# Kernel tuning notes

Measured on AMD Instinct MI355X. Metric: run time of the kernel, lower is better.

## Reference

```python
import jax, jax.numpy as jnp
import numpy as np

B, C, H, W = 2, 256, 64, 64
FEAT = 256          # in_channels * expansion_ratio
HEADS = 8
HS = FEAT // HEADS  # 32
OUT = 256


def setup_inputs() -> dict:
    key = jax.random.key(0)
    ks = jax.random.split(key, 12)
    inp = {
        "x": jax.random.normal(ks[0], (B, C, H, W), jnp.float32),
        "mod_multiplier": jax.random.normal(ks[1], (B, FEAT), jnp.float32),
        "mod_bias": jax.random.normal(ks[2], (B, FEAT), jnp.float32),
        # learned parameters (1x1 convs as matrices)
        "w_qkv": jax.random.normal(ks[3], (3 * FEAT, C), jnp.float32) * 0.02,
        "b_qkv": jnp.zeros((3 * FEAT,), jnp.float32),
        "w_proj": jax.random.normal(ks[4], (OUT, FEAT), jnp.float32) * 0.02,
        "pe_q_h": jax.random.normal(ks[5], (1, FEAT, H, 1), jnp.float32) * 0.02,
        "pe_q_w": jax.random.normal(ks[6], (1, FEAT, 1, W), jnp.float32) * 0.02,
        "pe_k_h": jax.random.normal(ks[7], (1, FEAT, H, 1), jnp.float32) * 0.02,
        "pe_k_w": jax.random.normal(ks[8], (1, FEAT, 1, W), jnp.float32) * 0.02,
        "pre_act_bias": jnp.zeros((1, C, 1, 1), jnp.float32),
        "pre_qkv_bias": jnp.zeros((1, C, 1, 1), jnp.float32),
        "pre_proj_bias": jnp.zeros((1, FEAT, 1, 1), jnp.float32),
        "id_scale": jnp.ones((1, OUT, 1, 1), jnp.float32),
    }
    return inp


def reference(x, mod_multiplier, mod_bias, w_qkv, b_qkv, w_proj,
              pe_q_h, pe_q_w, pe_k_h, pe_k_w,
              pre_act_bias, pre_qkv_bias, pre_proj_bias, id_scale):
    b = x.shape[0]
    # pre-activation (Fixup-style biases)
    x_preact = jax.nn.silu(x + pre_act_bias) + pre_qkv_bias
    # 1x1 conv -> QKV: [b, 3F, H, W]
    qkv = jnp.einsum('bchw,oc->bohw', x_preact, w_qkv) + b_qkv[None, :, None, None]
    q, k, v = jnp.split(qkv, 3, axis=1)
    # additive positional embeddings
    q = q + pe_q_h + pe_q_w
    k = k + pe_k_h + pe_k_w
    # FiLM modulation of query
    q = q * mod_multiplier[:, :, None, None] + mod_bias[:, :, None, None]
    # [b, heads, head_size, H*W]
    q = q.reshape(b, HEADS, HS, H * W)
    k = k.reshape(b, HEADS, HS, H * W)
    v = v.reshape(b, HEADS, HS, H * W)
    scale = jnp.asarray(HS ** 0.5, x.dtype)
    logits = jnp.einsum('bhdn,bhdm->bhnm', q, k) / scale
    weights = jax.nn.softmax(logits, axis=-1)
    attn = jnp.einsum('bhnm,bhdm->bhdn', weights, v)
    attn = attn.reshape(b, FEAT, H, W)
    # output projection (1x1 conv, no bias)
    x_res = jnp.einsum('bchw,oc->bohw', attn + pre_proj_bias, w_proj)
    return x * id_scale + x_res
```

## Files before the change

kernel.cpp:

```cpp
#include <hip/hip_runtime.h>
#include <hip/hip_bf16.h>
#include <cstdint>

#define NB   2
#define NC   256
#define NN   4096
#define NH   8
#define HSZ  32
#define NF   256
#define N3F  768

typedef __bf16 bf16x8 __attribute__((ext_vector_type(8)));
typedef __bf16 bf16x4 __attribute__((ext_vector_type(4)));
typedef short  s16x4  __attribute__((ext_vector_type(4)));
typedef float  floatx4 __attribute__((ext_vector_type(4)));

#define QSCALE 0.25506601622184f

__global__ void k_prep(const float* __restrict__ x, const float* __restrict__ pab,
                       const float* __restrict__ pqb, __bf16* __restrict__ y,
                       const float* __restrict__ wqkv, const float* __restrict__ wproj,
                       __bf16* __restrict__ wqb, __bf16* __restrict__ wpb) {
    __shared__ __bf16 ct[32 * 264];
    int bid = blockIdx.x, tid = threadIdx.x;
    if (bid >= 256) {
        int id = (bid - 256) * 1024 + tid * 4;
        const float* src = (id < 196608) ? (wqkv + id) : (wproj + (id - 196608));
        __bf16* dst = (id < 196608) ? (wqb + id) : (wpb + (id - 196608));
        float4 v = *(const float4*)src;
        bf16x4 o;
        o[0] = (__bf16)v.x; o[1] = (__bf16)v.y; o[2] = (__bf16)v.z; o[3] = (__bf16)v.w;
        *(bf16x4*)dst = o;
        return;
    }
    int b = bid >> 7, nt = bid & 127;
    int n0 = nt * 32;
    int cbase = tid >> 3, nc = tid & 7;
#pragma unroll
    for (int q = 0; q < 8; q++) {
        int c = cbase + q * 32;
        const float4 xv = *(const float4*)(x + ((size_t)b * NC + c) * NN + n0 + nc * 4);
        float bias = pab[c], qb = pqb[c];
        float vs[4] = {xv.x, xv.y, xv.z, xv.w};
#pragma unroll
        for (int i = 0; i < 4; i++) {
            float s = vs[i] + bias;
            float r = s / (1.f + __expf(-s)) + qb;
            ct[(nc * 4 + i) * 264 + c] = (__bf16)r;
        }
    }
    __syncthreads();
#pragma unroll
    for (int q = 0; q < 4; q++) {
        int id = tid + q * 256;
        int n = id >> 5, ck = (id & 31) * 8;
        bf16x8 v = *(const bf16x8*)(ct + n * 264 + ck);
        *(bf16x8*)(y + ((size_t)b * NN + n0 + n) * NC + ck) = v;
    }
}

__launch_bounds__(256)
__global__ void k_qkv(const __bf16* __restrict__ y, const __bf16* __restrict__ wb,
                      const float* __restrict__ bqkv,
                      const float* __restrict__ peqh, const float* __restrict__ peqw,
                      const float* __restrict__ pekh, const float* __restrict__ pekw,
                      const float* __restrict__ mm, const float* __restrict__ mb,
                      __bf16* __restrict__ qs, __bf16* __restrict__ kf, __bf16* __restrict__ vf) {
    __shared__ __bf16 smem[4][64 * 40];
    __bf16* ct = &smem[0][0];
    const int nt = blockIdx.x, ot = blockIdx.y, b = blockIdx.z;
    const int tid = threadIdx.x;
    const int wave = tid >> 6, lane = tid & 63, ln = lane & 15, quad = lane >> 4;
    const int wm = (wave & 1) * 32, wn = (wave >> 1) * 32;
    floatx4 acc[2][2];
#pragma unroll
    for (int i = 0; i < 2; i++)
#pragma unroll
        for (int j = 0; j < 2; j++) acc[i][j] = 0.f;
    const __bf16* ysrc = y + ((size_t)b * NN + nt * 64) * NC;
    const __bf16* wsrc = wb + (size_t)ot * 64 * NC;
    const int r0 = tid >> 2, c0 = (tid & 3) * 8;
    bf16x8 ya = *(const bf16x8*)(ysrc + (size_t)r0 * NC + c0);
    bf16x8 wa = *(const bf16x8*)(wsrc + (size_t)r0 * NC + c0);
    for (int ko = 0; ko < 8; ko++) {
        int buf = ko & 1;
        *(bf16x8*)(&smem[buf][r0 * 40 + c0]) = ya;
        *(bf16x8*)(&smem[2 + buf][r0 * 40 + c0]) = wa;
        __syncthreads();
        if (ko < 7) {
            int kc = (ko + 1) * 32;
            ya = *(const bf16x8*)(ysrc + (size_t)r0 * NC + kc + c0);
            wa = *(const bf16x8*)(wsrc + (size_t)r0 * NC + kc + c0);
        }
        bf16x8 af[2], bfr[2];
#pragma unroll
        for (int ii = 0; ii < 2; ii++) af[ii]  = *(const bf16x8*)(&smem[buf][(wm + ii * 16 + ln) * 40 + quad * 8]);
#pragma unroll
        for (int jj = 0; jj < 2; jj++) bfr[jj] = *(const bf16x8*)(&smem[2 + buf][(wn + jj * 16 + ln) * 40 + quad * 8]);
#pragma unroll
        for (int ii = 0; ii < 2; ii++)
#pragma unroll
            for (int jj = 0; jj < 2; jj++)
                acc[ii][jj] = __builtin_amdgcn_mfma_f32_16x16x32_bf16(af[ii], bfr[jj], acc[ii][jj], 0, 0, 0);
    }
    __syncthreads();
    if (ot < 8) {
#pragma unroll
        for (int ii = 0; ii < 2; ii++)
#pragma unroll
            for (int jj = 0; jj < 2; jj++) {
                int o_l = wn + jj * 16 + ln;
                int o_g = ot * 64 + o_l;
                float bq = bqkv[o_g];
#pragma unroll
                for (int r = 0; r < 4; r++) {
                    int n_l = wm + ii * 16 + quad * 4 + r;
                    float val = acc[ii][jj][r] + bq;
                    if (ot < 4) {
                        val += peqh[o_g * 64 + nt] + peqw[o_g * 64 + n_l];
                        val = val * mm[b * NF + o_g] + mb[b * NF + o_g];
                        val *= QSCALE;
                    } else {
                        int c = o_g - 256;
                        val += pekh[c * 64 + nt] + pekw[c * 64 + n_l];
                    }
                    ct[n_l * 72 + o_l] = (__bf16)val;
                }
            }
        __syncthreads();
#pragma unroll
        for (int q = 0; q < 2; q++) {
            int id = tid + q * 256;
            int n_l = id >> 3, oc = (id & 7) * 8;
            bf16x8 v = *(const bf16x8*)(ct + n_l * 72 + oc);
            int n_g = nt * 64 + n_l;
            int o_g = ot * 64 + oc;
            if (ot < 4) {
                int h = o_g >> 5, d = o_g & 31;
                *(bf16x8*)(qs + (((size_t)b * NH + h) * NN + n_g) * HSZ + d) = v;
            } else {
                int c = o_g - 256, h = c >> 5, d0 = c & 31;
                size_t blk = ((size_t)(b * NH + h) * 256 + (n_g >> 4)) * 512;
                *(bf16x8*)(kf + blk + (d0 >> 3) * 128 + (n_g & 15) * 8) = v;
            }
        }
    } else {
#pragma unroll
        for (int ii = 0; ii < 2; ii++)
#pragma unroll
            for (int jj = 0; jj < 2; jj++) {
                int o_l = wn + jj * 16 + ln;
                float bq = bqkv[ot * 64 + o_l];
#pragma unroll
                for (int r = 0; r < 4; r++) {
                    int n_l = wm + ii * 16 + quad * 4 + r;
                    ct[o_l * 72 + n_l] = (__bf16)(acc[ii][jj][r] + bq);
                }
            }
        __syncthreads();
#pragma unroll
        for (int q = 0; q < 4; q++) {
            int id = tid + q * 256;
            int o_l = id >> 4, ng4 = (id & 15) * 4;
            bf16x4 v = *(const bf16x4*)(ct + o_l * 72 + ng4);
            int c = (ot - 8) * 64 + o_l, h = c >> 5, d = c & 31;
            int dj = d >> 4, lnv = d & 15;
            int m_g = nt * 64 + ng4;
            size_t blk = ((size_t)(b * NH + h) * 256 + (m_g >> 4)) * 512;
            *(bf16x4*)(vf + blk + (((m_g >> 2) & 3) * 16 + lnv) * 8 + dj * 4) = v;
        }
    }
}

__launch_bounds__(256)
__global__ void k_attn(const __bf16* __restrict__ qs, const __bf16* __restrict__ kf,
                       const __bf16* __restrict__ vf,
                       __bf16* __restrict__ po, float* __restrict__ pl) {
    __shared__ __bf16 sbuf[2 * 8192];
    int bi = blockIdx.x;
    int xcd = bi & 7, r = bi >> 3;
    int bh = xcd * 2 + (r & 1);
    int r2 = r >> 1;
    int qt = r2 & 31, half = r2 >> 5;
    int tid = threadIdx.x, wave = tid >> 6, lane = tid & 63, ln = lane & 15, quad = lane >> 4;
    int n0 = qt * 128 + wave * 32;
    const __bf16* qbase = qs + (size_t)bh * NN * HSZ;
    const __bf16* kfb = kf + ((size_t)bh * 256 + half * 128) * 512;
    const __bf16* vfb = vf + ((size_t)bh * 256 + half * 128) * 512;
    bf16x8 qa[2];
    qa[0] = *(const bf16x8*)(qbase + (size_t)(n0 + ln) * HSZ + quad * 8);
    qa[1] = *(const bf16x8*)(qbase + (size_t)(n0 + 16 + ln) * HSZ + quad * 8);
    floatx4 o[2][2], o2[2];
    o[0][0] = 0.f; o[0][1] = 0.f; o[1][0] = 0.f; o[1][1] = 0.f;
    o2[0] = 0.f; o2[1] = 0.f;
    floatx4 zf = 0.f;
    s16x4 ones;
    ones[0] = (short)0x3F80; ones[1] = (short)0x3F80;
    ones[2] = (short)0x3F80; ones[3] = (short)0x3F80;
    const int toff = tid * 8;
    const int lo = lane * 8;
    bf16x8 kr0, kr1, vr0, vr1;
    kr0 = *(const bf16x8*)(kfb + toff);
    kr1 = *(const bf16x8*)(kfb + toff + 2048);
    vr0 = *(const bf16x8*)(vfb + toff);
    vr1 = *(const bf16x8*)(vfb + toff + 2048);
    for (int mt = 0; mt < 16; mt++) {
        int bo = (mt & 1) << 13;
        *(bf16x8*)(sbuf + bo + toff) = kr0;
        *(bf16x8*)(sbuf + bo + toff + 2048) = kr1;
        *(bf16x8*)(sbuf + bo + 4096 + toff) = vr0;
        *(bf16x8*)(sbuf + bo + 4096 + toff + 2048) = vr1;
        __syncthreads();
        if (mt < 15) {
            const __bf16* kn = kfb + (mt + 1) * 4096;
            const __bf16* vn = vfb + (mt + 1) * 4096;
            kr0 = *(const bf16x8*)(kn + toff);
            kr1 = *(const bf16x8*)(kn + toff + 2048);
            vr0 = *(const bf16x8*)(vn + toff);
            vr1 = *(const bf16x8*)(vn + toff + 2048);
        }
        const __bf16* kl = sbuf + bo;
        const __bf16* vl = sbuf + bo + 4096;
#pragma unroll
        for (int j = 0; j < 8; j++) {
            bf16x8 kfr = *(const bf16x8*)(kl + j * 512 + lo);
            bf16x8 vfr = *(const bf16x8*)(vl + j * 512 + lo);
            s16x4 vb0, vb1;
            __builtin_memcpy(&vb0, &vfr, 8);
            __builtin_memcpy(&vb1, (const char*)&vfr + 8, 8);
#pragma unroll
            for (int i = 0; i < 2; i++) {
                floatx4 s = __builtin_amdgcn_mfma_f32_16x16x32_bf16(kfr, qa[i], zf, 0, 0, 0);
                bf16x4 p;
#pragma unroll
                for (int rr = 0; rr < 4; rr++)
                    p[rr] = (__bf16)__builtin_amdgcn_exp2f(s[rr]);
                s16x4 pa;
                __builtin_memcpy(&pa, &p, 8);
                o[i][0] = __builtin_amdgcn_mfma_f32_16x16x16bf16_1k(pa, vb0, o[i][0], 0, 0, 0);
                o[i][1] = __builtin_amdgcn_mfma_f32_16x16x16bf16_1k(pa, vb1, o[i][1], 0, 0, 0);
                o2[i]   = __builtin_amdgcn_mfma_f32_16x16x16bf16_1k(pa, ones, o2[i], 0, 0, 0);
            }
        }
    }
    size_t plbase = (size_t)(half * 16 + bh) * NN;
    if (ln == 0)
#pragma unroll
        for (int i = 0; i < 2; i++)
#pragma unroll
            for (int rr = 0; rr < 4; rr++)
                pl[plbase + n0 + i * 16 + quad * 4 + rr] = o2[i][rr];
    __bf16* ct = sbuf;
#pragma unroll
    for (int i = 0; i < 2; i++)
#pragma unroll
        for (int dj = 0; dj < 2; dj++)
#pragma unroll
            for (int rr = 0; rr < 4; rr++)
                ct[(wave * 32 + i * 16 + quad * 4 + rr) * 32 + dj * 16 + ln] = (__bf16)o[i][dj][rr];
    __syncthreads();
    size_t pobase = ((size_t)(half * 16 + bh) * NN + (size_t)qt * 128) * HSZ;
#pragma unroll
    for (int q = 0; q < 2; q++) {
        int id = tid + q * 256;
        int n_l = id >> 2, dc = (id & 3) * 8;
        *(bf16x8*)(po + pobase + n_l * HSZ + dc) = *(const bf16x8*)(ct + n_l * 32 + dc);
    }
}

__launch_bounds__(256)
__global__ void k_proj(const __bf16* __restrict__ po, const float* __restrict__ pl,
                       const __bf16* __restrict__ wpb, const float* __restrict__ ppb,
                       const float* __restrict__ x, const float* __restrict__ idsc,
                       float* __restrict__ out) {
    __shared__ __bf16 at[64 * 264];
    __shared__ __bf16 bt[2][64 * 40];
    __shared__ float linv[8 * 64];
    __shared__ float ppbs[256];
    int nt = blockIdx.x, ot = blockIdx.y, b = blockIdx.z;
    int tid = threadIdx.x, wave = tid >> 6, lane = tid & 63, ln = lane & 15, quad = lane >> 4;
    int wo = (wave & 1) * 32, wn = (wave >> 1) * 32;
#pragma unroll
    for (int q = 0; q < 8; q++) {
        int id = tid + q * 256;
        int row = id >> 5, fc = (id & 31) * 8;
        *(bf16x8*)(at + row * 264 + fc) = *(const bf16x8*)(wpb + (size_t)(ot * 64 + row) * NF + fc);
    }
#pragma unroll
    for (int q = 0; q < 2; q++) {
        int id = tid + q * 256;
        int h = id >> 6, n_l = id & 63;
        size_t base = (size_t)(b * NH + h) * NN + nt * 64 + n_l;
        linv[id] = 1.f / (pl[base] + pl[base + (size_t)16 * NN]);
    }
    ppbs[tid] = ppb[tid];
    __syncthreads();
    floatx4 acc[2][2];
#pragma unroll
    for (int i = 0; i < 2; i++)
#pragma unroll
        for (int j = 0; j < 2; j++) acc[i][j] = 0.f;
    const int n_l = tid >> 2, dh8 = (tid & 3) * 8;
    const size_t hstep = (size_t)NN * HSZ;
    const size_t half_off = (size_t)16 * NN * HSZ;
    size_t prow = ((size_t)b * NH * NN + (size_t)nt * 64 + n_l) * HSZ + dh8;
    bf16x8 p0 = *(const bf16x8*)(po + prow);
    bf16x8 p1 = *(const bf16x8*)(po + prow + half_off);
    for (int ko = 0; ko < 8; ko++) {
        int buf = ko & 1;
        float iv = linv[ko * 64 + n_l];
        bf16x8 c;
#pragma unroll
        for (int e = 0; e < 8; e++)
            c[e] = (__bf16)(((float)p0[e] + (float)p1[e]) * iv + ppbs[ko * 32 + dh8 + e]);
        *(bf16x8*)(&bt[buf][n_l * 40 + dh8]) = c;
        __syncthreads();
        if (ko < 7) {
            size_t pr = prow + (size_t)(ko + 1) * hstep;
            p0 = *(const bf16x8*)(po + pr);
            p1 = *(const bf16x8*)(po + pr + half_off);
        }
        bf16x8 af[2], bfr[2];
#pragma unroll
        for (int oi = 0; oi < 2; oi++) af[oi]  = *(const bf16x8*)(at + (wo + oi * 16 + ln) * 264 + ko * 32 + quad * 8);
#pragma unroll
        for (int nj = 0; nj < 2; nj++) bfr[nj] = *(const bf16x8*)(&bt[buf][(wn + nj * 16 + ln) * 40 + quad * 8]);
#pragma unroll
        for (int oi = 0; oi < 2; oi++)
#pragma unroll
            for (int nj = 0; nj < 2; nj++)
                acc[oi][nj] = __builtin_amdgcn_mfma_f32_16x16x32_bf16(af[oi], bfr[nj], acc[oi][nj], 0, 0, 0);
    }
#pragma unroll
    for (int oi = 0; oi < 2; oi++)
#pragma unroll
        for (int nj = 0; nj < 2; nj++)
#pragma unroll
            for (int r = 0; r < 4; r++) {
                int o_g = ot * 64 + wo + oi * 16 + quad * 4 + r;
                int n_g = nt * 64 + wn + nj * 16 + ln;
                size_t idx = ((size_t)b * NF + o_g) * NN + n_g;
                out[idx] = x[idx] * idsc[o_g] + acc[oi][nj][r];
            }
}

extern "C" void kernel_launch(void* const* d_in, const int* in_sizes, int n_in,
                              void* d_out, int out_size, void* d_ws, size_t ws_size,
                              hipStream_t stream) {
    (void)in_sizes; (void)n_in; (void)out_size; (void)ws_size;
    const float* x    = (const float*)d_in[0];
    const float* mm   = (const float*)d_in[1];
    const float* mb   = (const float*)d_in[2];
    const float* wqkv = (const float*)d_in[3];
    const float* bqkv = (const float*)d_in[4];
    const float* wproj= (const float*)d_in[5];
    const float* peqh = (const float*)d_in[6];
    const float* peqw = (const float*)d_in[7];
    const float* pekh = (const float*)d_in[8];
    const float* pekw = (const float*)d_in[9];
    const float* pab  = (const float*)d_in[10];
    const float* pqb  = (const float*)d_in[11];
    const float* ppb  = (const float*)d_in[12];
    const float* idsc = (const float*)d_in[13];
    float* out = (float*)d_out;

    __bf16* ws = (__bf16*)d_ws;
    const size_t SEG = 2097152;
    __bf16* y    = ws;
    __bf16* qs   = ws + SEG;
    __bf16* kf   = ws + SEG * 2;
    __bf16* vf   = ws + SEG * 3;
    __bf16* po   = ws + SEG * 4;
    float*  pl   = (float*)(ws + SEG * 6);
    __bf16* wqb  = ws + SEG * 6 + 262144;
    __bf16* wpb  = wqb + 196608;

    hipLaunchKernelGGL(k_prep, dim3(512), dim3(256), 0, stream,
                       x, pab, pqb, y, wqkv, wproj, wqb, wpb);
    hipLaunchKernelGGL(k_qkv,  dim3(64, 12, 2), dim3(256), 0, stream,
                       y, wqb, bqkv, peqh, peqw, pekh, pekw, mm, mb, qs, kf, vf);
    hipLaunchKernelGGL(k_attn, dim3(1024), dim3(256), 0, stream, qs, kf, vf, po, pl);
    hipLaunchKernelGGL(k_proj, dim3(64, 4, 2), dim3(256), 0, stream,
                       po, pl, wpb, ppb, x, idsc, out);
}
```

Measured before the change: 175.0 us.

## Shrink attention LDS tiles, sum softmax denominators on VALU, widen projection blocks

After: 175.8 us. No clear change (+0.4%).

```diff
diff --git a/kernel.cpp b/kernel.cpp
--- a/kernel.cpp
+++ b/kernel.cpp
@@ -83,9 +83,9 @@
     bf16x8 ya = *(const bf16x8*)(ysrc + (size_t)r0 * NC + c0);
     bf16x8 wa = *(const bf16x8*)(wsrc + (size_t)r0 * NC + c0);
     for (int ko = 0; ko < 8; ko++) {
-        int buf = ko & 1;
-        *(bf16x8*)(&smem[buf][r0 * 40 + c0]) = ya;
-        *(bf16x8*)(&smem[2 + buf][r0 * 40 + c0]) = wa;
+        int bo = ko & 1;
+        *(bf16x8*)(&smem[bo][r0 * 40 + c0]) = ya;
+        *(bf16x8*)(&smem[2 + bo][r0 * 40 + c0]) = wa;
         __syncthreads();
         if (ko < 7) {
             int kc = (ko + 1) * 32;
@@ -94,9 +94,9 @@
         }
         bf16x8 af[2], bfr[2];
 #pragma unroll
-        for (int ii = 0; ii < 2; ii++) af[ii]  = *(const bf16x8*)(&smem[buf][(wm + ii * 16 + ln) * 40 + quad * 8]);
-#pragma unroll
-        for (int jj = 0; jj < 2; jj++) bfr[jj] = *(const bf16x8*)(&smem[2 + buf][(wn + jj * 16 + ln) * 40 + quad * 8]);
+        for (int ii = 0; ii < 2; ii++) af[ii]  = *(const bf16x8*)(&smem[bo][(wm + ii * 16 + ln) * 40 + quad * 8]);
+#pragma unroll
+        for (int jj = 0; jj < 2; jj++) bfr[jj] = *(const bf16x8*)(&smem[2 + bo][(wn + jj * 16 + ln) * 40 + quad * 8]);
 #pragma unroll
         for (int ii = 0; ii < 2; ii++)
 #pragma unroll
@@ -172,11 +172,11 @@
     }
 }
 
-__launch_bounds__(256)
+__launch_bounds__(256, 6)
 __global__ void k_attn(const __bf16* __restrict__ qs, const __bf16* __restrict__ kf,
                        const __bf16* __restrict__ vf,
                        __bf16* __restrict__ po, float* __restrict__ pl) {
-    __shared__ __bf16 sbuf[2 * 8192];
+    __shared__ __bf16 sbuf[2 * 4096];
     int bi = blockIdx.x;
     int xcd = bi & 7, r = bi >> 3;
     int bh = xcd * 2 + (r & 1);
@@ -190,39 +190,28 @@
     bf16x8 qa[2];
     qa[0] = *(const bf16x8*)(qbase + (size_t)(n0 + ln) * HSZ + quad * 8);
     qa[1] = *(const bf16x8*)(qbase + (size_t)(n0 + 16 + ln) * HSZ + quad * 8);
-    floatx4 o[2][2], o2[2];
+    floatx4 o[2][2];
     o[0][0] = 0.f; o[0][1] = 0.f; o[1][0] = 0.f; o[1][1] = 0.f;
-    o2[0] = 0.f; o2[1] = 0.f;
+    floatx4 lsum4[2];
+    lsum4[0] = 0.f; lsum4[1] = 0.f;
     floatx4 zf = 0.f;
-    s16x4 ones;
-    ones[0] = (short)0x3F80; ones[1] = (short)0x3F80;
-    ones[2] = (short)0x3F80; ones[3] = (short)0x3F80;
     const int toff = tid * 8;
     const int lo = lane * 8;
-    bf16x8 kr0, kr1, vr0, vr1;
-    kr0 = *(const bf16x8*)(kfb + toff);
-    kr1 = *(const bf16x8*)(kfb + toff + 2048);
-    vr0 = *(const bf16x8*)(vfb + toff);
-    vr1 = *(const bf16x8*)(vfb + toff + 2048);
-    for (int mt = 0; mt < 16; mt++) {
-        int bo = (mt & 1) << 13;
-        *(bf16x8*)(sbuf + bo + toff) = kr0;
-        *(bf16x8*)(sbuf + bo + toff + 2048) = kr1;
-        *(bf16x8*)(sbuf + bo + 4096 + toff) = vr0;
-        *(bf16x8*)(sbuf + bo + 4096 + toff + 2048) = vr1;
-        __syncthreads();
-        if (mt < 15) {
-            const __bf16* kn = kfb + (mt + 1) * 4096;
-            const __bf16* vn = vfb + (mt + 1) * 4096;
-            kr0 = *(const bf16x8*)(kn + toff);
-            kr1 = *(const bf16x8*)(kn + toff + 2048);
-            vr0 = *(const bf16x8*)(vn + toff);
-            vr1 = *(const bf16x8*)(vn + toff + 2048);
+    bf16x8 kr = *(const bf16x8*)(kfb + toff);
+    bf16x8 vr = *(const bf16x8*)(vfb + toff);
+    for (int mt = 0; mt < 32; mt++) {
+        int bo = (mt & 1) << 12;
+        *(bf16x8*)(sbuf + bo + toff) = kr;
+        *(bf16x8*)(sbuf + bo + 2048 + toff) = vr;
+        __syncthreads();
+        if (mt < 31) {
+            kr = *(const bf16x8*)(kfb + (mt + 1) * 2048 + toff);
+            vr = *(const bf16x8*)(vfb + (mt + 1) * 2048 + toff);
         }
         const __bf16* kl = sbuf + bo;
-        const __bf16* vl = sbuf + bo + 4096;
-#pragma unroll
-        for (int j = 0; j < 8; j++) {
+        const __bf16* vl = sbuf + bo + 2048;
+#pragma unroll
+        for (int j = 0; j < 4; j++) {
             bf16x8 kfr = *(const bf16x8*)(kl + j * 512 + lo);
             bf16x8 vfr = *(const bf16x8*)(vl + j * 512 + lo);
             s16x4 vb0, vb1;
@@ -233,23 +222,26 @@
                 floatx4 s = __builtin_amdgcn_mfma_f32_16x16x32_bf16(kfr, qa[i], zf, 0, 0, 0);
                 bf16x4 p;
 #pragma unroll
-                for (int rr = 0; rr < 4; rr++)
-                    p[rr] = (__bf16)__builtin_amdgcn_exp2f(s[rr]);
+                for (int rr = 0; rr < 4; rr++) {
+                    float e = __builtin_amdgcn_exp2f(s[rr]);
+                    lsum4[i][rr] += e;
+                    p[rr] = (__bf16)e;
+                }
                 s16x4 pa;
                 __builtin_memcpy(&pa, &p, 8);
                 o[i][0] = __builtin_amdgcn_mfma_f32_16x16x16bf16_1k(pa, vb0, o[i][0], 0, 0, 0);
                 o[i][1] = __builtin_amdgcn_mfma_f32_16x16x16bf16_1k(pa, vb1, o[i][1], 0, 0, 0);
-                o2[i]   = __builtin_amdgcn_mfma_f32_16x16x16bf16_1k(pa, ones, o2[i], 0, 0, 0);
             }
         }
     }
     size_t plbase = (size_t)(half * 16 + bh) * NN;
-    if (ln == 0)
-#pragma unroll
-        for (int i = 0; i < 2; i++)
-#pragma unroll
-            for (int rr = 0; rr < 4; rr++)
-                pl[plbase + n0 + i * 16 + quad * 4 + rr] = o2[i][rr];
+#pragma unroll
+    for (int i = 0; i < 2; i++) {
+        float ls = lsum4[i][0] + lsum4[i][1] + lsum4[i][2] + lsum4[i][3];
+        ls += __shfl_xor(ls, 16, 64);
+        ls += __shfl_xor(ls, 32, 64);
+        if (quad == 0) pl[plbase + n0 + i * 16 + ln] = ls;
+    }
     __bf16* ct = sbuf;
 #pragma unroll
     for (int i = 0; i < 2; i++)
@@ -268,7 +260,7 @@
     }
 }
 
-__launch_bounds__(256)
+__launch_bounds__(512)
 __global__ void k_proj(const __bf16* __restrict__ po, const float* __restrict__ pl,
                        const __bf16* __restrict__ wpb, const float* __restrict__ ppb,
                        const float* __restrict__ x, const float* __restrict__ idsc,
@@ -279,69 +271,59 @@
     __shared__ float ppbs[256];
     int nt = blockIdx.x, ot = blockIdx.y, b = blockIdx.z;
     int tid = threadIdx.x, wave = tid >> 6, lane = tid & 63, ln = lane & 15, quad = lane >> 4;
-    int wo = (wave & 1) * 32, wn = (wave >> 1) * 32;
-#pragma unroll
-    for (int q = 0; q < 8; q++) {
-        int id = tid + q * 256;
+    int wo = (wave & 1) * 32, wn = (wave >> 1) * 16;
+#pragma unroll
+    for (int q = 0; q < 4; q++) {
+        int id = tid + q * 512;
         int row = id >> 5, fc = (id & 31) * 8;
         *(bf16x8*)(at + row * 264 + fc) = *(const bf16x8*)(wpb + (size_t)(ot * 64 + row) * NF + fc);
     }
-#pragma unroll
-    for (int q = 0; q < 2; q++) {
-        int id = tid + q * 256;
-        int h = id >> 6, n_l = id & 63;
+    {
+        int h = tid >> 6, n_l = tid & 63;
         size_t base = (size_t)(b * NH + h) * NN + nt * 64 + n_l;
-        linv[id] = 1.f / (pl[base] + pl[base + (size_t)16 * NN]);
-    }
-    ppbs[tid] = ppb[tid];
+        linv[tid] = 1.f / (pl[base] + pl[base + (size_t)16 * NN]);
+        if (tid < 256) ppbs[tid] = ppb[tid];
+    }
     __syncthreads();
-    floatx4 acc[2][2];
-#pragma unroll
-    for (int i = 0; i < 2; i++)
-#pragma unroll
-        for (int j = 0; j < 2; j++) acc[i][j] = 0.f;
-    const int n_l = tid >> 2, dh8 = (tid & 3) * 8;
+    floatx4 acc[2];
+    acc[0] = 0.f; acc[1] = 0.f;
+    const int n_l = tid >> 3, dh4 = (tid & 7) * 4;
     const size_t hstep = (size_t)NN * HSZ;
     const size_t half_off = (size_t)16 * NN * HSZ;
-    size_t prow = ((size_t)b * NH * NN + (size_t)nt * 64 + n_l) * HSZ + dh8;
-    bf16x8 p0 = *(const bf16x8*)(po + prow);
-    bf16x8 p1 = *(const bf16x8*)(po + prow + half_off);
+    size_t prow = ((size_t)b * NH * NN + (size_t)nt * 64 + n_l) * HSZ + dh4;
+    bf16x4 p0 = *(const bf16x4*)(po + prow);
+    bf16x4 p1 = *(const bf16x4*)(po + prow + half_off);
     for (int ko = 0; ko < 8; ko++) {
         int buf = ko & 1;
         float iv = linv[ko * 64 + n_l];
-        bf16x8 c;
-#pragma unroll
-        for (int e = 0; e < 8; e++)
-            c[e] = (__bf16)(((float)p0[e] + (float)p1[e]) * iv + ppbs[ko * 32 + dh8 + e]);
-        *(bf16x8*)(&bt[buf][n_l * 40 + dh8]) = c;
+        bf16x4 c;
+#pragma unroll
+        for (int e = 0; e < 4; e++)
+            c[e] = (__bf16)(((float)p0[e] + (float)p1[e]) * iv + ppbs[ko * 32 + dh4 + e]);
+        *(bf16x4*)(&bt[buf][n_l * 40 + dh4]) = c;
         __syncthreads();
         if (ko < 7) {
             size_t pr = prow + (size_t)(ko + 1) * hstep;
-            p0 = *(const bf16x8*)(po + pr);
-            p1 = *(const bf16x8*)(po + pr + half_off);
-        }
-        bf16x8 af[2], bfr[2];
-#pragma unroll
-        for (int oi = 0; oi < 2; oi++) af[oi]  = *(const bf16x8*)(at + (wo + oi * 16 + ln) * 264 + ko * 32 + quad * 8);
-#pragma unroll
-        for (int nj = 0; nj < 2; nj++) bfr[nj] = *(const bf16x8*)(&bt[buf][(wn + nj * 16 + ln) * 40 + quad * 8]);
+            p0 = *(const bf16x4*)(po + pr);
+            p1 = *(const bf16x4*)(po + pr + half_off);
+        }
+        bf16x8 af[2], bfr;
+#pragma unroll
+        for (int oi = 0; oi < 2; oi++) af[oi] = *(const bf16x8*)(at + (wo + oi * 16 + ln) * 264 + ko * 32 + quad * 8);
+        bfr = *(const bf16x8*)(&bt[buf][(wn + ln) * 40 + quad * 8]);
 #pragma unroll
         for (int oi = 0; oi < 2; oi++)
-#pragma unroll
-            for (int nj = 0; nj < 2; nj++)
-                acc[oi][nj] = __builtin_amdgcn_mfma_f32_16x16x32_bf16(af[oi], bfr[nj], acc[oi][nj], 0, 0, 0);
+            acc[oi] = __builtin_amdgcn_mfma_f32_16x16x32_bf16(af[oi], bfr, acc[oi], 0, 0, 0);
     }
 #pragma unroll
     for (int oi = 0; oi < 2; oi++)
 #pragma unroll
-        for (int nj = 0; nj < 2; nj++)
-#pragma unroll
-            for (int r = 0; r < 4; r++) {
-                int o_g = ot * 64 + wo + oi * 16 + quad * 4 + r;
-                int n_g = nt * 64 + wn + nj * 16 + ln;
-                size_t idx = ((size_t)b * NF + o_g) * NN + n_g;
-                out[idx] = x[idx] * idsc[o_g] + acc[oi][nj][r];
-            }
+        for (int r = 0; r < 4; r++) {
+            int o_g = ot * 64 + wo + oi * 16 + quad * 4 + r;
+            int n_g = nt * 64 + wn + ln;
+            size_t idx = ((size_t)b * NF + o_g) * NN + n_g;
+            out[idx] = x[idx] * idsc[o_g] + acc[oi][r];
+        }
 }
 
 extern "C" void kernel_launch(void* const* d_in, const int* in_sizes, int n_in,
@@ -380,6 +362,6 @@
     hipLaunchKernelGGL(k_qkv,  dim3(64, 12, 2), dim3(256), 0, stream,
                        y, wqb, bqkv, peqh, peqw, pekh, pekw, mm, mb, qs, kf, vf);
     hipLaunchKernelGGL(k_attn, dim3(1024), dim3(256), 0, stream, qs, kf, vf, po, pl);
-    hipLaunchKernelGGL(k_proj, dim3(64, 4, 2), dim3(256), 0, stream,
+    hipLaunchKernelGGL(k_proj, dim3(64, 4, 2), dim3(512), 0, stream,
                        po, pl, wpb, ppb, x, idsc, out);
 }
```
